# Kernel tuning notes

Hardware: AMD Instinct MI355X
Metric: run time of the kernel (lower is better)

Reference implementation:

```python
import jax, jax.numpy as jnp
import numpy as np

N = 100000
E = 800000
IN = 64
HID = 32
H1 = 4
G = 256  # num graphs
OUT = 1
NEG_SLOPE = 0.2


def setup_inputs() -> dict:
    key = jax.random.key(0)
    ks = jax.random.split(key, 16)
    x = jax.random.normal(ks[0], (N, IN), dtype=jnp.float32)
    edge_index = jax.random.randint(ks[1], (2, E), 0, N, dtype=jnp.int64)
    batch = jnp.sort(jax.random.randint(ks[2], (N,), 0, G, dtype=jnp.int64))

    def xavier(k, shape):
        fan_in, fan_out = shape[0], shape[1]
        lim = float(np.sqrt(6.0 / (fan_in + fan_out)))
        return jax.random.uniform(k, shape, jnp.float32, -lim, lim)

    # GATv2 layer 1: in=IN, out=HID, heads=H1
    Wl1 = xavier(ks[3], (IN, H1 * HID)); bl1 = jnp.zeros((H1 * HID,), jnp.float32)
    Wr1 = xavier(ks[4], (IN, H1 * HID)); br1 = jnp.zeros((H1 * HID,), jnp.float32)
    att1 = xavier(ks[5], (H1, HID))
    bias1 = jnp.zeros((H1 * HID,), jnp.float32)
    # GATv2 layer 2: in=H1*HID, out=HID, heads=1
    Wl2 = xavier(ks[6], (H1 * HID, HID)); bl2 = jnp.zeros((HID,), jnp.float32)
    Wr2 = xavier(ks[7], (H1 * HID, HID)); br2 = jnp.zeros((HID,), jnp.float32)
    att2 = xavier(ks[8], (1, HID))
    bias2 = jnp.zeros((HID,), jnp.float32)
    # head MLP
    Wh1 = xavier(ks[9], (HID, HID)); bh1 = jnp.zeros((HID,), jnp.float32)
    Wh2 = xavier(ks[10], (HID, OUT)); bh2 = jnp.zeros((OUT,), jnp.float32)
    return dict(x=x, edge_index=edge_index, batch=batch,
                Wl1=Wl1, bl1=bl1, Wr1=Wr1, br1=br1, att1=att1, bias1=bias1,
                Wl2=Wl2, bl2=bl2, Wr2=Wr2, br2=br2, att2=att2, bias2=bias2,
                Wh1=Wh1, bh1=bh1, Wh2=Wh2, bh2=bh2)


def gatv2_conv(x, src, dst, Wl, bl, Wr, br, att, bias, heads, out_ch):
    n = x.shape[0]
    xl = (x @ Wl + bl).reshape(n, heads, out_ch)  # source transform (x_j)
    xr = (x @ Wr + br).reshape(n, heads, out_ch)  # target transform (x_i)
    e = jax.nn.leaky_relu(xl[src] + xr[dst], NEG_SLOPE)        # [E,H,C]
    alpha = jnp.einsum('ehc,hc->eh', e, att)                    # [E,H]
    amax = jax.ops.segment_max(alpha, dst, num_segments=n)      # [N,H]
    ea = jnp.exp(alpha - amax[dst])
    denom = jax.ops.segment_sum(ea, dst, num_segments=n)
    a = ea / (denom[dst] + 1e-16)                               # softmax per dst node
    out = jax.ops.segment_sum(xl[src] * a[:, :, None], dst, num_segments=n)
    return out.reshape(n, heads * out_ch) + bias


def reference(x, edge_index, batch,
              Wl1, bl1, Wr1, br1, att1, bias1,
              Wl2, bl2, Wr2, br2, att2, bias2,
              Wh1, bh1, Wh2, bh2):
    n = x.shape[0]
    # add self-loops (PyG GATv2Conv default)
    loops = jnp.arange(n, dtype=edge_index.dtype)
    src = jnp.concatenate([edge_index[0], loops])
    dst = jnp.concatenate([edge_index[1], loops])

    h = gatv2_conv(x, src, dst, Wl1, bl1, Wr1, br1, att1, bias1, H1, HID)
    h = jax.nn.celu(h, alpha=1.0)
    # dropout: identity in eval mode
    h = gatv2_conv(h, src, dst, Wl2, bl2, Wr2, br2, att2, bias2, 1, HID)

    # global mean pool over graphs
    sums = jax.ops.segment_sum(h, batch, num_segments=G)          # [G,HID]
    counts = jax.ops.segment_sum(jnp.ones((n,), h.dtype), batch, num_segments=G)
    pooled = sums / jnp.maximum(counts, 1.0)[:, None]

    z = jax.nn.relu(pooled @ Wh1 + bh1)
    return z @ Wh2 + bh2  # [G, OUT]
```

## Files before the change

### kernel.cpp

```cpp
#include <hip/hip_runtime.h>
#include <hip/hip_fp16.h>
#include <math.h>

#define NN 100000
#define NE 800000
#define ET (NN + NE)
#define NG 256
#define SLOPE 0.2f
#define LOG2E 1.44269504088896340736f
#define NB1 ((NN + 255) / 256)
#define NRT 6250

typedef _Float16 f16x2 __attribute__((ext_vector_type(2)));
typedef _Float16 f16x8 __attribute__((ext_vector_type(8)));
typedef float    f32x4 __attribute__((ext_vector_type(4)));

__device__ __forceinline__ void unpack8(float4 raw, float* x) {
    const __half2* hp = (const __half2*)&raw;
    #pragma unroll
    for (int j = 0; j < 4; ++j) {
        float2 f = __half22float2(hp[j]);
        x[2 * j] = f.x; x[2 * j + 1] = f.y;
    }
}
__device__ __forceinline__ void unpack4(float2 raw, float* x) {
    const __half2* hp = (const __half2*)&raw;
    #pragma unroll
    for (int j = 0; j < 2; ++j) {
        float2 f = __half22float2(hp[j]);
        x[2 * j] = f.x; x[2 * j + 1] = f.y;
    }
}

template<int K, int MT, int MHALF>
__global__ void packW_kernel(const float* __restrict__ Wl, const float* __restrict__ Wr,
                             __half* __restrict__ hi, __half* __restrict__ lo)
{
    constexpr int KS  = K / 32;
    constexpr int TOT = (MT / 16) * KS * 64 * 8;
    for (int idx = blockIdx.x * 256 + threadIdx.x; idx < TOT; idx += gridDim.x * 256) {
        const int i   = idx & 7;
        const int l   = (idx >> 3) & 63;
        const int rem = idx >> 9;
        const int ks  = rem % KS;
        const int ct  = rem / KS;
        const int k   = ks * 32 + (l >> 4) * 8 + i;
        const int col = ct * 16 + (l & 15);
        const float w = (col < MHALF) ? Wl[(size_t)k * MHALF + col]
                                      : Wr[(size_t)k * MHALF + (col - MHALF)];
        const __half h = __float2half(w);
        hi[idx] = h;
        lo[idx] = __float2half(w - __half2float(h));
    }
}

__global__ __launch_bounds__(256, 4)
void t1_mfma_kernel(const float* __restrict__ X,
                    const __half* __restrict__ Whi, const __half* __restrict__ Wlo,
                    const float* __restrict__ bl, const float* __restrict__ br,
                    __half* __restrict__ XLh, __half* __restrict__ XRh)
{
    const int rt = blockIdx.x * 4 + (threadIdx.x >> 6);
    if (rt >= NRT) return;
    const int l = threadIdx.x & 63;
    const int row_a = rt * 16 + (l & 15);
    const int kbase = (l >> 4) * 8;

    f16x8 a[2];
    #pragma unroll
    for (int ks = 0; ks < 2; ++ks) {
        const float4 x0 = *(const float4*)(X + (size_t)row_a * 64 + ks * 32 + kbase);
        const float4 x1 = *(const float4*)(X + (size_t)row_a * 64 + ks * 32 + kbase + 4);
        a[ks][0] = (_Float16)x0.x; a[ks][1] = (_Float16)x0.y;
        a[ks][2] = (_Float16)x0.z; a[ks][3] = (_Float16)x0.w;
        a[ks][4] = (_Float16)x1.x; a[ks][5] = (_Float16)x1.y;
        a[ks][6] = (_Float16)x1.z; a[ks][7] = (_Float16)x1.w;
    }

    for (int ct = 0; ct < 16; ++ct) {
        f32x4 acc = {0.f, 0.f, 0.f, 0.f};
        #pragma unroll
        for (int ks = 0; ks < 2; ++ks) {
            const f16x8 bh = *(const f16x8*)(Whi + ((size_t)(ct * 2 + ks) * 64 + l) * 8);
            const f16x8 bL = *(const f16x8*)(Wlo + ((size_t)(ct * 2 + ks) * 64 + l) * 8);
            acc = __builtin_amdgcn_mfma_f32_16x16x32_f16(a[ks], bh, acc, 0, 0, 0);
            acc = __builtin_amdgcn_mfma_f32_16x16x32_f16(a[ks], bL, acc, 0, 0, 0);
        }
        const int col = ct * 16 + (l & 15);
        const float bias = (col < 128) ? bl[col] : br[col - 128];
        __half* const dst = (col < 128) ? XLh : XRh;
        const int dcol = col & 127;
        #pragma unroll
        for (int r = 0; r < 4; ++r) {
            const int row = rt * 16 + (l >> 4) * 4 + r;
            dst[(size_t)row * 128 + dcol] = __float2half(acc[r] + bias);
        }
    }
}

__global__ __launch_bounds__(256, 4)
void t2_mfma_kernel(const __half* __restrict__ H1h,
                    const __half* __restrict__ Whi, const __half* __restrict__ Wlo,
                    const float* __restrict__ bl, const float* __restrict__ br,
                    __half* __restrict__ XLh, __half* __restrict__ XRh)
{
    const int rt = blockIdx.x * 4 + (threadIdx.x >> 6);
    if (rt >= NRT) return;
    const int l = threadIdx.x & 63;
    const int row_a = rt * 16 + (l & 15);
    const int kbase = (l >> 4) * 8;

    f16x8 a[4];
    #pragma unroll
    for (int ks = 0; ks < 4; ++ks)
        a[ks] = *(const f16x8*)(H1h + (size_t)row_a * 128 + ks * 32 + kbase);

    for (int ct = 0; ct < 4; ++ct) {
        f32x4 acc = {0.f, 0.f, 0.f, 0.f};
        #pragma unroll
        for (int ks = 0; ks < 4; ++ks) {
            const f16x8 bh = *(const f16x8*)(Whi + ((size_t)(ct * 4 + ks) * 64 + l) * 8);
            const f16x8 bL = *(const f16x8*)(Wlo + ((size_t)(ct * 4 + ks) * 64 + l) * 8);
            acc = __builtin_amdgcn_mfma_f32_16x16x32_f16(a[ks], bh, acc, 0, 0, 0);
            acc = __builtin_amdgcn_mfma_f32_16x16x32_f16(a[ks], bL, acc, 0, 0, 0);
        }
        const int col = ct * 16 + (l & 15);
        const float bias = (col < 32) ? bl[col] : br[col - 32];
        __half* const dst = (col < 32) ? XLh : XRh;
        const int dcol = col & 31;
        #pragma unroll
        for (int r = 0; r < 4; ++r) {
            const int row = rt * 16 + (l >> 4) * 4 + r;
            dst[(size_t)row * 32 + dcol] = __float2half(acc[r] + bias);
        }
    }
}

__global__ void hist_kernel(const int* __restrict__ edst, int* __restrict__ deg)
{
    int e = blockIdx.x * 256 + threadIdx.x;
    if (e >= ET) return;
    int d = (e < NE) ? edst[e] : (e - NE);
    atomicAdd(deg + d, 1);
}

__global__ void scan1_kernel(const int* __restrict__ deg, int* __restrict__ rowstart,
                             int* __restrict__ bsum)
{
    __shared__ int lds[256];
    int t = threadIdx.x, idx = blockIdx.x * 256 + t;
    int v = (idx < NN) ? deg[idx] : 0;
    lds[t] = v;
    __syncthreads();
    #pragma unroll
    for (int off = 1; off < 256; off <<= 1) {
        int add = (t >= off) ? lds[t - off] : 0;
        __syncthreads();
        lds[t] += add;
        __syncthreads();
    }
    if (idx < NN) rowstart[idx + 1] = lds[t];
    if (t == 255) bsum[blockIdx.x] = lds[255];
}

__global__ void scan2_kernel(int* __restrict__ bsum)
{
    __shared__ int lds[512];
    int t = threadIdx.x;
    int v = (t < NB1) ? bsum[t] : 0;
    lds[t] = v;
    __syncthreads();
    #pragma unroll
    for (int off = 1; off < 512; off <<= 1) {
        int add = (t >= off) ? lds[t - off] : 0;
        __syncthreads();
        lds[t] += add;
        __syncthreads();
    }
    if (t < NB1) bsum[t] = lds[t] - v;
}

__global__ void scan3_kernel(int* __restrict__ rowstart, const int* __restrict__ bsum)
{
    int idx = blockIdx.x * 256 + threadIdx.x;
    if (idx == 0) rowstart[0] = 0;
    if (idx < NN) rowstart[idx + 1] += bsum[blockIdx.x];
}

__global__ void scatter_kernel(const int* __restrict__ esrc, const int* __restrict__ edst,
                               const int* __restrict__ rowstart,
                               int* __restrict__ cursor, int* __restrict__ csr_src)
{
    int e = blockIdx.x * 256 + threadIdx.x;
    if (e >= ET) return;
    int s, d;
    if (e < NE) { s = esrc[e]; d = edst[e]; } else { s = e - NE; d = s; }
    int pos = rowstart[d] + atomicAdd(cursor + d, 1);
    csr_src[pos] = s;
}

__global__ void gat1_kernel(const int* __restrict__ rowstart, const int* __restrict__ csr_src,
                            const __half* __restrict__ XLh, const __half* __restrict__ XRh,
                            const float* __restrict__ att, const float* __restrict__ bias,
                            __half* __restrict__ H1h)
{
    const int node = blockIdx.x * 4 + (threadIdx.x >> 6);
    if (node >= NN) return;
    const int lane = threadIdx.x & 63;
    const int slot = lane >> 4;
    const int q    = lane & 15;
    const int c0   = q * 8;

    float4 xr_raw = *(const float4*)(XRh + (size_t)node * 128 + c0);
    const f16x2* xrh = (const f16x2*)&xr_raw;
    f16x2 ath[4];
    {
        const float4 a0 = *(const float4*)(att + c0);
        const float4 a1 = *(const float4*)(att + c0 + 4);
        ath[0] = (f16x2){(_Float16)(a0.x * LOG2E), (_Float16)(a0.y * LOG2E)};
        ath[1] = (f16x2){(_Float16)(a0.z * LOG2E), (_Float16)(a0.w * LOG2E)};
        ath[2] = (f16x2){(_Float16)(a1.x * LOG2E), (_Float16)(a1.y * LOG2E)};
        ath[3] = (f16x2){(_Float16)(a1.z * LOG2E), (_Float16)(a1.w * LOG2E)};
    }
    const f16x2 s2 = {(_Float16)SLOPE, (_Float16)SLOPE};
    const int beg = rowstart[node], end = rowstart[node + 1];
    float m = -INFINITY, ssum = 0.f;
    float acc[8] = {0.f, 0.f, 0.f, 0.f, 0.f, 0.f, 0.f, 0.f};

    for (int i = beg; i < end; i += 4) {
        const int idx    = i + slot;
        const bool valid = idx < end;
        const int s = valid ? csr_src[idx] : 0;
        float4 xl_raw = *(const float4*)(XLh + (size_t)s * 128 + c0);
        const f16x2* xlh = (const f16x2*)&xl_raw;
        float p = 0.f;
        #pragma unroll
        for (int j = 0; j < 4; ++j) {
            f16x2 v  = xlh[j] + xrh[j];
            f16x2 lv = __builtin_elementwise_max(v, s2 * v);
            p = __builtin_amdgcn_fdot2(lv, ath[j], p, false);
        }
        p += __shfl_xor(p, 1);
        p += __shfl_xor(p, 2);
        if (!valid) p = -INFINITY;
        float pm = fmaxf(p, __shfl_xor(p, 16));
        pm = fmaxf(pm, __shfl_xor(pm, 32));
        if (__any(pm > m + 8.f)) {
            const float mn = fmaxf(m, pm);
            const float sc = exp2f(m - mn);
            ssum *= sc;
            #pragma unroll
            for (int j = 0; j < 8; ++j) acc[j] *= sc;
            m = mn;
        }
        const float e = exp2f(p - m);
        ssum += e;
        float xlf[8];
        unpack8(xl_raw, xlf);
        #pragma unroll
        for (int j = 0; j < 8; ++j)
            acc[j] = fmaf(e, xlf[j], acc[j]);
    }
    ssum += __shfl_xor(ssum, 16);
    ssum += __shfl_xor(ssum, 32);
    #pragma unroll
    for (int j = 0; j < 8; ++j) {
        acc[j] += __shfl_xor(acc[j], 16);
        acc[j] += __shfl_xor(acc[j], 32);
    }
    if (slot == 0) {
        const float inv = 1.f / (ssum + 1e-16f);
        const float4 b0 = *(const float4*)(bias + c0);
        const float4 b1 = *(const float4*)(bias + c0 + 4);
        const float bb[8] = {b0.x, b0.y, b0.z, b0.w, b1.x, b1.y, b1.z, b1.w};
        __half2 outh[4];
        #pragma unroll
        for (int j = 0; j < 4; ++j) {
            float o0 = acc[2 * j] * inv + bb[2 * j];
            float o1 = acc[2 * j + 1] * inv + bb[2 * j + 1];
            o0 = o0 > 0.f ? o0 : expm1f(o0);
            o1 = o1 > 0.f ? o1 : expm1f(o1);
            outh[j] = __float22half2_rn(make_float2(o0, o1));
        }
        *(float4*)(H1h + (size_t)node * 128 + c0) = *(const float4*)outh;
    }
}

__global__ void gat2_kernel(const int* __restrict__ rowstart, const int* __restrict__ csr_src,
                            const __half* __restrict__ XLh, const __half* __restrict__ XRh,
                            const float* __restrict__ att,
                            float* __restrict__ H2)
{
    const int node = blockIdx.x * 8 + (threadIdx.x >> 5);
    if (node >= NN) return;
    const int l2   = threadIdx.x & 31;
    const int slot = l2 >> 3;
    const int q    = l2 & 7;
    const int c0   = q * 4;

    float2 xr_raw = *(const float2*)(XRh + (size_t)node * 32 + c0);
    const f16x2* xrh = (const f16x2*)&xr_raw;
    f16x2 ath[2];
    {
        const float4 a = *(const float4*)(att + c0);
        ath[0] = (f16x2){(_Float16)(a.x * LOG2E), (_Float16)(a.y * LOG2E)};
        ath[1] = (f16x2){(_Float16)(a.z * LOG2E), (_Float16)(a.w * LOG2E)};
    }
    const f16x2 s2 = {(_Float16)SLOPE, (_Float16)SLOPE};
    const int beg = rowstart[node], end = rowstart[node + 1];
    float m = -INFINITY, ssum = 0.f;
    float acc[4] = {0.f, 0.f, 0.f, 0.f};

    for (int i = beg; i < end; i += 4) {
        const int idx    = i + slot;
        const bool valid = idx < end;
        const int s = valid ? csr_src[idx] : 0;
        float2 xl_raw = *(const float2*)(XLh + (size_t)s * 32 + c0);
        const f16x2* xlh = (const f16x2*)&xl_raw;
        float p = 0.f;
        #pragma unroll
        for (int j = 0; j < 2; ++j) {
            f16x2 v  = xlh[j] + xrh[j];
            f16x2 lv = __builtin_elementwise_max(v, s2 * v);
            p = __builtin_amdgcn_fdot2(lv, ath[j], p, false);
        }
        p += __shfl_xor(p, 1);
        p += __shfl_xor(p, 2);
        p += __shfl_xor(p, 4);
        if (!valid) p = -INFINITY;
        float pm = fmaxf(p, __shfl_xor(p, 8));
        pm = fmaxf(pm, __shfl_xor(pm, 16));
        if (__any(pm > m + 8.f)) {
            const float mn = fmaxf(m, pm);
            const float sc = exp2f(m - mn);
            ssum *= sc;
            #pragma unroll
            for (int j = 0; j < 4; ++j) acc[j] *= sc;
            m = mn;
        }
        const float e = exp2f(p - m);
        ssum += e;
        float xlf[4];
        unpack4(xl_raw, xlf);
        #pragma unroll
        for (int j = 0; j < 4; ++j)
            acc[j] = fmaf(e, xlf[j], acc[j]);
    }
    ssum += __shfl_xor(ssum, 8);
    ssum += __shfl_xor(ssum, 16);
    #pragma unroll
    for (int j = 0; j < 4; ++j) {
        acc[j] += __shfl_xor(acc[j], 8);
        acc[j] += __shfl_xor(acc[j], 16);
    }
    if (slot == 0) {
        const float inv = 1.f / (ssum + 1e-16f);
        float4 o;
        o.x = acc[0] * inv; o.y = acc[1] * inv;
        o.z = acc[2] * inv; o.w = acc[3] * inv;
        *(float4*)(H2 + (size_t)node * 32 + c0) = o;
    }
}

__global__ void pool_kernel(const float* __restrict__ h2, const float* __restrict__ bias2,
                            const int* __restrict__ batch,
                            float* __restrict__ pool, float* __restrict__ cnt)
{
    const int c    = threadIdx.x & 31;
    const int slot = threadIdx.x >> 5;
    const int base = blockIdx.x * 256;
    const float b = bias2[c];
    float acc = 0.f, cacc = 0.f;
    int curg = -1;
    for (int i = slot; i < 256; i += 8) {
        int node = base + i;
        if (node >= NN) break;
        int g = batch[node];
        if (g != curg) {
            if (curg >= 0) {
                atomicAdd(pool + (size_t)curg * 32 + c, acc);
                if (c == 0) atomicAdd(cnt + curg, cacc);
            }
            acc = 0.f; cacc = 0.f; curg = g;
        }
        acc += h2[(size_t)node * 32 + c] + b;
        cacc += 1.f;
    }
    if (curg >= 0) {
        atomicAdd(pool + (size_t)curg * 32 + c, acc);
        if (c == 0) atomicAdd(cnt + curg, cacc);
    }
}

__global__ void head_kernel(const float* __restrict__ pool, const float* __restrict__ cnt,
                            const float* __restrict__ Wh1, const float* __restrict__ bh1,
                            const float* __restrict__ Wh2, const float* __restrict__ bh2,
                            float* __restrict__ out)
{
    int g = blockIdx.x;
    int c = threadIdx.x;
    float partial = 0.f;
    if (c < 32) {
        float invc = 1.f / fmaxf(cnt[g], 1.f);
        float acc = bh1[c];
        #pragma unroll
        for (int k = 0; k < 32; ++k)
            acc = fmaf(pool[g * 32 + k] * invc, Wh1[k * 32 + c], acc);
        float z = fmaxf(acc, 0.f);
        partial = z * Wh2[c];
    }
    #pragma unroll
    for (int off = 32; off >= 1; off >>= 1)
        partial += __shfl_down(partial, off);
    if (c == 0) out[g] = partial + bh2[0];
}

extern "C" void kernel_launch(void* const* d_in, const int* in_sizes, int n_in,
                              void* d_out, int out_size, void* d_ws, size_t ws_size,
                              hipStream_t stream)
{
    const float* x     = (const float*)d_in[0];
    const int*   ei    = (const int*)d_in[1];
    const int*   batch = (const int*)d_in[2];
    const float* Wl1   = (const float*)d_in[3];
    const float* bl1   = (const float*)d_in[4];
    const float* Wr1   = (const float*)d_in[5];
    const float* br1   = (const float*)d_in[6];
    const float* att1  = (const float*)d_in[7];
    const float* bias1 = (const float*)d_in[8];
    const float* Wl2   = (const float*)d_in[9];
    const float* bl2   = (const float*)d_in[10];
    const float* Wr2   = (const float*)d_in[11];
    const float* br2   = (const float*)d_in[12];
    const float* att2  = (const float*)d_in[13];
    const float* bias2 = (const float*)d_in[14];
    const float* Wh1   = (const float*)d_in[15];
    const float* bh1   = (const float*)d_in[16];
    const float* Wh2   = (const float*)d_in[17];
    const float* bh2   = (const float*)d_in[18];
    const int* esrc = ei;
    const int* edst = ei + NE;

    char* wsb = (char*)d_ws;
    __half* xl1h = (__half*)wsb;
    __half* xr1h = (__half*)(wsb + (size_t)NN * 128 * 2);
    __half* h1h  = xr1h;
    char* p2 = wsb + (size_t)NN * 128 * 4;
    __half* xl2h = (__half*)p2;
    __half* xr2h = (__half*)(p2 + (size_t)NN * 32 * 2);
    float*  h2   = (float*)(p2 + (size_t)NN * 32 * 4);
    float*  pool = (float*)(p2 + (size_t)NN * 32 * 8);
    float*  cnt  = pool + (size_t)NG * 32;
    int* ib       = (int*)(cnt + NG);
    int* deg      = ib;
    int* rowstart = ib + NN;
    int* bsum     = ib + 2 * NN + 1;
    int* csr_src  = ib + 2 * NN + 1 + 512;
    __half* whi1  = (__half*)(csr_src + ET);
    __half* wlo1  = whi1 + 16384;
    __half* whi2  = wlo1 + 16384;
    __half* wlo2  = whi2 + 8192;

    hipMemsetAsync(deg, 0, NN * sizeof(int), stream);
    hipMemsetAsync(pool, 0, (size_t)(NG * 33) * sizeof(float), stream);
    packW_kernel<64, 256, 128><<<64, 256, 0, stream>>>(Wl1, Wr1, whi1, wlo1);
    packW_kernel<128, 64, 32><<<32, 256, 0, stream>>>(Wl2, Wr2, whi2, wlo2);
    hist_kernel<<<(ET + 255) / 256, 256, 0, stream>>>(edst, deg);
    scan1_kernel<<<NB1, 256, 0, stream>>>(deg, rowstart, bsum);
    scan2_kernel<<<1, 512, 0, stream>>>(bsum);
    scan3_kernel<<<NB1, 256, 0, stream>>>(rowstart, bsum);
    hipMemsetAsync(deg, 0, NN * sizeof(int), stream);
    scatter_kernel<<<(ET + 255) / 256, 256, 0, stream>>>(esrc, edst, rowstart, deg, csr_src);

    t1_mfma_kernel<<<(NRT + 3) / 4, 256, 0, stream>>>(
        x, whi1, wlo1, bl1, br1, xl1h, xr1h);
    gat1_kernel<<<(NN + 3) / 4, 256, 0, stream>>>(
        rowstart, csr_src, xl1h, xr1h, att1, bias1, h1h);

    t2_mfma_kernel<<<(NRT + 3) / 4, 256, 0, stream>>>(
        h1h, whi2, wlo2, bl2, br2, xl2h, xr2h);
    gat2_kernel<<<(NN + 7) / 8, 256, 0, stream>>>(
        rowstart, csr_src, xl2h, xr2h, att2, h2);

    pool_kernel<<<(NN + 255) / 256, 256, 0, stream>>>(h2, bias2, batch, pool, cnt);
    head_kernel<<<NG, 64, 0, stream>>>(pool, cnt, Wh1, bh1, Wh2, bh2, (float*)d_out);
}
```

Baseline: 282.0 us.

## Widen per-lane feature slices to process more edges per wave, merge memsets

In both GAT aggregation kernels each lane now covers twice as many channels: 16 halves in layer 1 and 8 in layer 2. Twice as many edges (8 slots instead of 4) are processed per wave iteration, which halves loop trips for typical degrees and cuts per-edge shuffle reductions. The CSR scatter now uses a separate zeroed cursor array, so the deg, cursor and pool buffers are cleared in one memset instead of three. The cost is more registers per lane and more padded idle slots for low-degree nodes.

Result: slower. 319.4 us (+13.3%).

```diff
diff --git a/kernel.cpp b/kernel.cpp
--- a/kernel.cpp
+++ b/kernel.cpp
@@ -19,14 +19,6 @@
     const __half2* hp = (const __half2*)&raw;
     #pragma unroll
     for (int j = 0; j < 4; ++j) {
-        float2 f = __half22float2(hp[j]);
-        x[2 * j] = f.x; x[2 * j + 1] = f.y;
-    }
-}
-__device__ __forceinline__ void unpack4(float2 raw, float* x) {
-    const __half2* hp = (const __half2*)&raw;
-    #pragma unroll
-    for (int j = 0; j < 2; ++j) {
         float2 f = __half22float2(hp[j]);
         x[2 * j] = f.x; x[2 * j + 1] = f.y;
     }
@@ -207,44 +199,157 @@
     const int node = blockIdx.x * 4 + (threadIdx.x >> 6);
     if (node >= NN) return;
     const int lane = threadIdx.x & 63;
-    const int slot = lane >> 4;
-    const int q    = lane & 15;
-    const int c0   = q * 8;
-
-    float4 xr_raw = *(const float4*)(XRh + (size_t)node * 128 + c0);
-    const f16x2* xrh = (const f16x2*)&xr_raw;
-    f16x2 ath[4];
+    const int slot = lane >> 3;
+    const int q    = lane & 7;
+    const int c0   = q * 16;
+
+    f16x2 xrp[8];
     {
-        const float4 a0 = *(const float4*)(att + c0);
-        const float4 a1 = *(const float4*)(att + c0 + 4);
-        ath[0] = (f16x2){(_Float16)(a0.x * LOG2E), (_Float16)(a0.y * LOG2E)};
-        ath[1] = (f16x2){(_Float16)(a0.z * LOG2E), (_Float16)(a0.w * LOG2E)};
-        ath[2] = (f16x2){(_Float16)(a1.x * LOG2E), (_Float16)(a1.y * LOG2E)};
-        ath[3] = (f16x2){(_Float16)(a1.z * LOG2E), (_Float16)(a1.w * LOG2E)};
+        float4 xr_a = *(const float4*)(XRh + (size_t)node * 128 + c0);
+        float4 xr_b = *(const float4*)(XRh + (size_t)node * 128 + c0 + 8);
+        const f16x2* pa = (const f16x2*)&xr_a;
+        const f16x2* pb = (const f16x2*)&xr_b;
+        #pragma unroll
+        for (int j = 0; j < 4; ++j) { xrp[j] = pa[j]; xrp[4 + j] = pb[j]; }
+    }
+    f16x2 ath[8];
+    #pragma unroll
+    for (int jj = 0; jj < 4; ++jj) {
+        const float4 a = *(const float4*)(att + c0 + jj * 4);
+        ath[2 * jj]     = (f16x2){(_Float16)(a.x * LOG2E), (_Float16)(a.y * LOG2E)};
+        ath[2 * jj + 1] = (f16x2){(_Float16)(a.z * LOG2E), (_Float16)(a.w * LOG2E)};
     }
     const f16x2 s2 = {(_Float16)SLOPE, (_Float16)SLOPE};
     const int beg = rowstart[node], end = rowstart[node + 1];
     float m = -INFINITY, ssum = 0.f;
-    float acc[8] = {0.f, 0.f, 0.f, 0.f, 0.f, 0.f, 0.f, 0.f};
-
-    for (int i = beg; i < end; i += 4) {
+    float acc[16];
+    #pragma unroll
+    for (int j = 0; j < 16; ++j) acc[j] = 0.f;
+
+    for (int i = beg; i < end; i += 8) {
         const int idx    = i + slot;
         const bool valid = idx < end;
         const int s = valid ? csr_src[idx] : 0;
-        float4 xl_raw = *(const float4*)(XLh + (size_t)s * 128 + c0);
-        const f16x2* xlh = (const f16x2*)&xl_raw;
+        float4 xa = *(const float4*)(XLh + (size_t)s * 128 + c0);
+        float4 xb = *(const float4*)(XLh + (size_t)s * 128 + c0 + 8);
+        const f16x2* pa = (const f16x2*)&xa;
+        const f16x2* pb = (const f16x2*)&xb;
         float p = 0.f;
         #pragma unroll
         for (int j = 0; j < 4; ++j) {
-            f16x2 v  = xlh[j] + xrh[j];
+            f16x2 v  = pa[j] + xrp[j];
+            f16x2 lv = __builtin_elementwise_max(v, s2 * v);
+            p = __builtin_amdgcn_fdot2(lv, ath[j], p, false);
+        }
+        #pragma unroll
+        for (int j = 0; j < 4; ++j) {
+            f16x2 v  = pb[j] + xrp[4 + j];
+            f16x2 lv = __builtin_elementwise_max(v, s2 * v);
+            p = __builtin_amdgcn_fdot2(lv, ath[4 + j], p, false);
+        }
+        p += __shfl_xor(p, 1);
+        if (!valid) p = -INFINITY;
+        float pm = fmaxf(p, __shfl_xor(p, 8));
+        pm = fmaxf(pm, __shfl_xor(pm, 16));
+        pm = fmaxf(pm, __shfl_xor(pm, 32));
+        if (__any(pm > m + 8.f)) {
+            const float mn = fmaxf(m, pm);
+            const float sc = exp2f(m - mn);
+            ssum *= sc;
+            #pragma unroll
+            for (int j = 0; j < 16; ++j) acc[j] *= sc;
+            m = mn;
+        }
+        const float e = exp2f(p - m);
+        ssum += e;
+        float xlf[16];
+        unpack8(xa, xlf);
+        unpack8(xb, xlf + 8);
+        #pragma unroll
+        for (int j = 0; j < 16; ++j)
+            acc[j] = fmaf(e, xlf[j], acc[j]);
+    }
+    #pragma unroll
+    for (int d = 8; d <= 32; d <<= 1) {
+        ssum += __shfl_xor(ssum, d);
+        #pragma unroll
+        for (int j = 0; j < 16; ++j) acc[j] += __shfl_xor(acc[j], d);
+    }
+    if (slot == 0) {
+        const float inv = 1.f / (ssum + 1e-16f);
+        float bb[16];
+        #pragma unroll
+        for (int jj = 0; jj < 4; ++jj) {
+            const float4 b = *(const float4*)(bias + c0 + jj * 4);
+            bb[4 * jj] = b.x; bb[4 * jj + 1] = b.y;
+            bb[4 * jj + 2] = b.z; bb[4 * jj + 3] = b.w;
+        }
+        __half2 outh[8];
+        #pragma unroll
+        for (int j = 0; j < 8; ++j) {
+            float o0 = acc[2 * j] * inv + bb[2 * j];
+            float o1 = acc[2 * j + 1] * inv + bb[2 * j + 1];
+            o0 = o0 > 0.f ? o0 : expm1f(o0);
+            o1 = o1 > 0.f ? o1 : expm1f(o1);
+            outh[j] = __float22half2_rn(make_float2(o0, o1));
+        }
+        *(float4*)(H1h + (size_t)node * 128 + c0)     = ((const float4*)outh)[0];
+        *(float4*)(H1h + (size_t)node * 128 + c0 + 8) = ((const float4*)outh)[1];
+    }
+}
+
+__global__ void gat2_kernel(const int* __restrict__ rowstart, const int* __restrict__ csr_src,
+                            const __half* __restrict__ XLh, const __half* __restrict__ XRh,
+                            const float* __restrict__ att,
+                            float* __restrict__ H2)
+{
+    const int node = blockIdx.x * 8 + (threadIdx.x >> 5);
+    if (node >= NN) return;
+    const int l2   = threadIdx.x & 31;
+    const int slot = l2 >> 2;
+    const int q    = l2 & 3;
+    const int c0   = q * 8;
+
+    f16x2 xrp[4];
+    {
+        float4 xr_raw = *(const float4*)(XRh + (size_t)node * 32 + c0);
+        const f16x2* pr = (const f16x2*)&xr_raw;
+        #pragma unroll
+        for (int j = 0; j < 4; ++j) xrp[j] = pr[j];
+    }
+    f16x2 ath[4];
+    #pragma unroll
+    for (int jj = 0; jj < 2; ++jj) {
+        const float4 a = *(const float4*)(att + c0 + jj * 4);
+        ath[2 * jj]     = (f16x2){(_Float16)(a.x * LOG2E), (_Float16)(a.y * LOG2E)};
+        ath[2 * jj + 1] = (f16x2){(_Float16)(a.z * LOG2E), (_Float16)(a.w * LOG2E)};
+    }
+    const f16x2 s2 = {(_Float16)SLOPE, (_Float16)SLOPE};
+    const int beg = rowstart[node], end = rowstart[node + 1];
+    float m = -INFINITY, ssum = 0.f;
+    float acc[8];
+    #pragma unroll
+    for (int j = 0; j < 8; ++j) acc[j] = 0.f;
+
+    for (int i = beg; i < end; i += 8) {
+        const int idx    = i + slot;
+        const bool valid = idx < end;
+        const int s = valid ? csr_src[idx] : 0;
+        float4 xl_raw = *(const float4*)(XLh + (size_t)s * 32 + c0);
+        const f16x2* pl = (const f16x2*)&xl_raw;
+        float p = 0.f;
+        #pragma unroll
+        for (int j = 0; j < 4; ++j) {
+            f16x2 v  = pl[j] + xrp[j];
             f16x2 lv = __builtin_elementwise_max(v, s2 * v);
             p = __builtin_amdgcn_fdot2(lv, ath[j], p, false);
         }
         p += __shfl_xor(p, 1);
         p += __shfl_xor(p, 2);
         if (!valid) p = -INFINITY;
-        float pm = fmaxf(p, __shfl_xor(p, 16));
-        pm = fmaxf(pm, __shfl_xor(pm, 32));
+        float pm = fmaxf(p, __shfl_xor(p, 4));
+        pm = fmaxf(pm, __shfl_xor(pm, 8));
+        pm = fmaxf(pm, __shfl_xor(pm, 16));
         if (__any(pm > m + 8.f)) {
             const float mn = fmaxf(m, pm);
             const float sc = exp2f(m - mn);
@@ -261,104 +366,19 @@
         for (int j = 0; j < 8; ++j)
             acc[j] = fmaf(e, xlf[j], acc[j]);
     }
-    ssum += __shfl_xor(ssum, 16);
-    ssum += __shfl_xor(ssum, 32);
-    #pragma unroll
-    for (int j = 0; j < 8; ++j) {
-        acc[j] += __shfl_xor(acc[j], 16);
-        acc[j] += __shfl_xor(acc[j], 32);
+    #pragma unroll
+    for (int d = 4; d <= 16; d <<= 1) {
+        ssum += __shfl_xor(ssum, d);
+        #pragma unroll
+        for (int j = 0; j < 8; ++j) acc[j] += __shfl_xor(acc[j], d);
     }
     if (slot == 0) {
         const float inv = 1.f / (ssum + 1e-16f);
-        const float4 b0 = *(const float4*)(bias + c0);
-        const float4 b1 = *(const float4*)(bias + c0 + 4);
-        const float bb[8] = {b0.x, b0.y, b0.z, b0.w, b1.x, b1.y, b1.z, b1.w};
-        __half2 outh[4];
-        #pragma unroll
-        for (int j = 0; j < 4; ++j) {
-            float o0 = acc[2 * j] * inv + bb[2 * j];
-            float o1 = acc[2 * j + 1] * inv + bb[2 * j + 1];
-            o0 = o0 > 0.f ? o0 : expm1f(o0);
-            o1 = o1 > 0.f ? o1 : expm1f(o1);
-            outh[j] = __float22half2_rn(make_float2(o0, o1));
-        }
-        *(float4*)(H1h + (size_t)node * 128 + c0) = *(const float4*)outh;
-    }
-}
-
-__global__ void gat2_kernel(const int* __restrict__ rowstart, const int* __restrict__ csr_src,
-                            const __half* __restrict__ XLh, const __half* __restrict__ XRh,
-                            const float* __restrict__ att,
-                            float* __restrict__ H2)
-{
-    const int node = blockIdx.x * 8 + (threadIdx.x >> 5);
-    if (node >= NN) return;
-    const int l2   = threadIdx.x & 31;
-    const int slot = l2 >> 3;
-    const int q    = l2 & 7;
-    const int c0   = q * 4;
-
-    float2 xr_raw = *(const float2*)(XRh + (size_t)node * 32 + c0);
-    const f16x2* xrh = (const f16x2*)&xr_raw;
-    f16x2 ath[2];
-    {
-        const float4 a = *(const float4*)(att + c0);
-        ath[0] = (f16x2){(_Float16)(a.x * LOG2E), (_Float16)(a.y * LOG2E)};
-        ath[1] = (f16x2){(_Float16)(a.z * LOG2E), (_Float16)(a.w * LOG2E)};
-    }
-    const f16x2 s2 = {(_Float16)SLOPE, (_Float16)SLOPE};
-    const int beg = rowstart[node], end = rowstart[node + 1];
-    float m = -INFINITY, ssum = 0.f;
-    float acc[4] = {0.f, 0.f, 0.f, 0.f};
-
-    for (int i = beg; i < end; i += 4) {
-        const int idx    = i + slot;
-        const bool valid = idx < end;
-        const int s = valid ? csr_src[idx] : 0;
-        float2 xl_raw = *(const float2*)(XLh + (size_t)s * 32 + c0);
-        const f16x2* xlh = (const f16x2*)&xl_raw;
-        float p = 0.f;
-        #pragma unroll
-        for (int j = 0; j < 2; ++j) {
-            f16x2 v  = xlh[j] + xrh[j];
-            f16x2 lv = __builtin_elementwise_max(v, s2 * v);
-            p = __builtin_amdgcn_fdot2(lv, ath[j], p, false);
-        }
-        p += __shfl_xor(p, 1);
-        p += __shfl_xor(p, 2);
-        p += __shfl_xor(p, 4);
-        if (!valid) p = -INFINITY;
-        float pm = fmaxf(p, __shfl_xor(p, 8));
-        pm = fmaxf(pm, __shfl_xor(pm, 16));
-        if (__any(pm > m + 8.f)) {
-            const float mn = fmaxf(m, pm);
-            const float sc = exp2f(m - mn);
-            ssum *= sc;
-            #pragma unroll
-            for (int j = 0; j < 4; ++j) acc[j] *= sc;
-            m = mn;
-        }
-        const float e = exp2f(p - m);
-        ssum += e;
-        float xlf[4];
-        unpack4(xl_raw, xlf);
-        #pragma unroll
-        for (int j = 0; j < 4; ++j)
-            acc[j] = fmaf(e, xlf[j], acc[j]);
-    }
-    ssum += __shfl_xor(ssum, 8);
-    ssum += __shfl_xor(ssum, 16);
-    #pragma unroll
-    for (int j = 0; j < 4; ++j) {
-        acc[j] += __shfl_xor(acc[j], 8);
-        acc[j] += __shfl_xor(acc[j], 16);
-    }
-    if (slot == 0) {
-        const float inv = 1.f / (ssum + 1e-16f);
-        float4 o;
-        o.x = acc[0] * inv; o.y = acc[1] * inv;
-        o.z = acc[2] * inv; o.w = acc[3] * inv;
-        *(float4*)(H2 + (size_t)node * 32 + c0) = o;
+        float4 o0, o1;
+        o0.x = acc[0] * inv; o0.y = acc[1] * inv; o0.z = acc[2] * inv; o0.w = acc[3] * inv;
+        o1.x = acc[4] * inv; o1.y = acc[5] * inv; o1.z = acc[6] * inv; o1.w = acc[7] * inv;
+        *(float4*)(H2 + (size_t)node * 32 + c0)     = o0;
+        *(float4*)(H2 + (size_t)node * 32 + c0 + 4) = o1;
     }
 }
 
@@ -449,28 +469,27 @@
     __half* xl2h = (__half*)p2;
     __half* xr2h = (__half*)(p2 + (size_t)NN * 32 * 2);
     float*  h2   = (float*)(p2 + (size_t)NN * 32 * 4);
-    float*  pool = (float*)(p2 + (size_t)NN * 32 * 8);
-    float*  cnt  = pool + (size_t)NG * 32;
-    int* ib       = (int*)(cnt + NG);
-    int* deg      = ib;
-    int* rowstart = ib + NN;
-    int* bsum     = ib + 2 * NN + 1;
-    int* csr_src  = ib + 2 * NN + 1 + 512;
-    __half* whi1  = (__half*)(csr_src + ET);
-    __half* wlo1  = whi1 + 16384;
-    __half* whi2  = wlo1 + 16384;
-    __half* wlo2  = whi2 + 8192;
-
-    hipMemsetAsync(deg, 0, NN * sizeof(int), stream);
-    hipMemsetAsync(pool, 0, (size_t)(NG * 33) * sizeof(float), stream);
+    int*    zr     = (int*)(p2 + (size_t)NN * 32 * 8);
+    int*    deg    = zr;
+    int*    cursor = zr + NN;
+    float*  pool   = (float*)(zr + 2 * NN);
+    float*  cnt    = pool + (size_t)NG * 32;
+    int* rowstart  = (int*)(cnt + NG);
+    int* bsum      = rowstart + NN + 1;
+    int* csr_src   = bsum + 512;
+    __half* whi1   = (__half*)(csr_src + ET);
+    __half* wlo1   = whi1 + 16384;
+    __half* whi2   = wlo1 + 16384;
+    __half* wlo2   = whi2 + 8192;
+
+    hipMemsetAsync(zr, 0, (size_t)(2 * NN + NG * 32 + NG) * sizeof(int), stream);
     packW_kernel<64, 256, 128><<<64, 256, 0, stream>>>(Wl1, Wr1, whi1, wlo1);
     packW_kernel<128, 64, 32><<<32, 256, 0, stream>>>(Wl2, Wr2, whi2, wlo2);
     hist_kernel<<<(ET + 255) / 256, 256, 0, stream>>>(edst, deg);
     scan1_kernel<<<NB1, 256, 0, stream>>>(deg, rowstart, bsum);
     scan2_kernel<<<1, 512, 0, stream>>>(bsum);
     scan3_kernel<<<NB1, 256, 0, stream>>>(rowstart, bsum);
-    hipMemsetAsync(deg, 0, NN * sizeof(int), stream);
-    scatter_kernel<<<(ET + 255) / 256, 256, 0, stream>>>(esrc, edst, rowstart, deg, csr_src);
+    scatter_kernel<<<(ET + 255) / 256, 256, 0, stream>>>(esrc, edst, rowstart, cursor, csr_src);
 
     t1_mfma_kernel<<<(NRT + 3) / 4, 256, 0, stream>>>(
         x, whi1, wlo1, bl1, br1, xl1h, xr1h);
```
